# Kernel optimization log

Hardware: AMD Instinct MI355X
Metric: run time of the kernel (lower is better)

The kernel has to match this reference:

```python
import jax, jax.numpy as jnp
import numpy as np

B, K, D = 8, 256, 768      # batch, num proposals, appearance_feature_dim
DK = 96                    # key_feature_dim
DG = 96                    # geo_feature_dim
NR = 8                     # n_relations (NR*DK == D required by residual add)


def setup_inputs() -> dict:
    key = jax.random.key(0)
    ks = jax.random.split(key, 10)
    s = 0.02
    return {
        "f_a": jax.random.normal(ks[0], (B, K, D), jnp.float32),
        "position_embedding": jax.random.uniform(ks[1], (B, K, K, DG), jnp.float32),
        # stacked per-head parameters (NR heads)
        "WG_w": jax.random.normal(ks[2], (NR, DG), jnp.float32) * s,
        "WG_b": jnp.zeros((NR,), jnp.float32),
        "WK_w": jax.random.normal(ks[3], (NR, D, DK), jnp.float32) * s,
        "WK_b": jnp.zeros((NR, DK), jnp.float32),
        "WQ_w": jax.random.normal(ks[4], (NR, D, DK), jnp.float32) * s,
        "WQ_b": jnp.zeros((NR, DK), jnp.float32),
        "WV_w": jax.random.normal(ks[5], (NR, D, DK), jnp.float32) * s,
        "WV_b": jnp.zeros((NR, DK), jnp.float32),
    }


def reference(f_a, position_embedding, WG_w, WG_b, WK_w, WK_b, WQ_w, WQ_b, WV_w, WV_b):
    # Per-head projections, all heads at once: [B, H, K, DK]
    k = jnp.einsum('bkd,hde->bhke', f_a, WK_w) + WK_b[:, None, :]
    q = jnp.einsum('bkd,hde->bhke', f_a, WQ_w) + WQ_b[:, None, :]
    v = jnp.einsum('bkd,hde->bhke', f_a, WV_w) + WV_b[:, None, :]
    # scaled_dot[b,h,m,n] = <k_m, q_n> / sqrt(DK)  (matches w_k.view(B,K,1,dk)*w_q.view(B,1,K,dk))
    scores = jnp.einsum('bhme,bhne->bhmn', k, q) * (1.0 / np.sqrt(DK)).astype(np.float32)
    # geometric bias: relu(WG(pe)) -> [B,H,K,K]
    w_g = jax.nn.relu(jnp.einsum('bmng,hg->bhmn', position_embedding, WG_w) + WG_b[:, None, None])
    logits = jnp.log(jnp.clip(w_g, 1e-6)) + scores
    # torch Softmax(dim=1) on [B,K,K] -> normalize over m axis (axis=2 here)
    attn = jax.nn.softmax(logits, axis=2)
    # output[b,n,:] = sum_m attn[b,h,m,n] * v[b,h,m,:], heads concatenated on feature dim
    out = jnp.einsum('bhmn,bhmd->bnhd', attn, v).reshape(f_a.shape[0], f_a.shape[1], -1)
    return out + f_a  # concat + f_a residual from RelationalProposalModule
```

## Files before the change

### kernel.cpp

```cpp
#include <hip/hip_runtime.h>

#define DD   768
#define NH   8
#define DKh  96

typedef __attribute__((ext_vector_type(8))) short short8;
typedef __attribute__((ext_vector_type(4))) float f32x4;

__device__ __forceinline__ unsigned short f2bf(float x) {
    union { float f; unsigned int u; } v; v.f = x;
    unsigned int r = v.u + 0x7FFFu + ((v.u >> 16) & 1u);
    return (unsigned short)(r >> 16);
}

__global__ __launch_bounds__(256) void k_cvt_a(const float* __restrict__ fa,
                                               unsigned short* __restrict__ abf) {
    int idx = blockIdx.x * 256 + threadIdx.x;
    float4 v = ((const float4*)fa)[idx];
    ushort4 o;
    o.x = f2bf(v.x); o.y = f2bf(v.y); o.z = f2bf(v.z); o.w = f2bf(v.w);
    ((ushort4*)abf)[idx] = o;
}

__global__ __launch_bounds__(256) void k_cvt_w(const float* __restrict__ wk,
                                               const float* __restrict__ wq,
                                               const float* __restrict__ wv,
                                               unsigned short* __restrict__ wbf) {
    __shared__ float ls[64 * 97];
    int pid = blockIdx.x / 12;
    int db  = blockIdx.x % 12;
    int p = pid >> 3, h = pid & 7;
    const float* src = (p == 0 ? wk : p == 1 ? wq : wv) + h * DD * DKh + db * 64 * DKh;
    int t = threadIdx.x;
#pragma unroll
    for (int i = 0; i < 24; ++i) {
        int f = t + 256 * i;
        int dl = f / 96, e = f - dl * 96;
        ls[dl * 97 + e] = src[f];
    }
    __syncthreads();
    unsigned short* dst = wbf + (p * 768 + h * 96) * DD + db * 64;
#pragma unroll
    for (int i = 0; i < 24; ++i) {
        int f = t + 256 * i;
        int e = f >> 6, dl = f & 63;
        dst[e * DD + dl] = f2bf(ls[dl * 97 + e]);
    }
}

__global__ __launch_bounds__(256) void k_proj(const unsigned short* __restrict__ abf,
                                              const unsigned short* __restrict__ wbf,
                                              const float* __restrict__ wkb,
                                              const float* __restrict__ wqb,
                                              const float* __restrict__ wvb,
                                              unsigned short* __restrict__ kb,
                                              unsigned short* __restrict__ qb,
                                              unsigned short* __restrict__ vt) {
    int w = threadIdx.x >> 6, lane = threadIdx.x & 63;
    int lrow = lane & 15, quad = lane >> 4;
    int rt = blockIdx.x / 36, cg = blockIdx.x % 36;
    int r0 = rt * 64 + w * 16;
    int c0 = cg * 64;
    f32x4 z = {0.f, 0.f, 0.f, 0.f};
    f32x4 acc[4] = {z, z, z, z};
    for (int kk = 0; kk < DD; kk += 32) {
        short8 a = *(const short8*)(abf + (r0 + lrow) * DD + kk + quad * 8);
#pragma unroll
        for (int tt = 0; tt < 4; ++tt) {
            short8 b = *(const short8*)(wbf + (c0 + tt * 16 + lrow) * DD + kk + quad * 8);
            acc[tt] = __builtin_amdgcn_mfma_f32_16x16x32_bf16(a, b, acc[tt], 0, 0, 0);
        }
    }
    int rbase = r0 + quad * 4;
    int b_ = rbase >> 8, mbase = rbase & 255;
#pragma unroll
    for (int tt = 0; tt < 4; ++tt) {
        int cc = c0 + tt * 16 + lrow;
        int p = cc / 768, rm = cc - p * 768;
        int h = rm / 96,  e = rm - h * 96;
        float bias = (p == 0 ? wkb : p == 1 ? wqb : wvb)[h * 96 + e];
        if (p == 2) {
            ushort4 v4;
            v4.x = f2bf(acc[tt][0] + bias);
            v4.y = f2bf(acc[tt][1] + bias);
            v4.z = f2bf(acc[tt][2] + bias);
            v4.w = f2bf(acc[tt][3] + bias);
            *(ushort4*)(vt + ((b_ * 8 + h) * 96 + e) * 256 + mbase) = v4;
        } else {
            float sc = (p == 1) ? 0.10206207261596577f : 1.0f;
            unsigned short* dst = (p == 0 ? kb : qb) + ((b_ * 8 + h) * 256 + mbase) * 96 + e;
#pragma unroll
            for (int r = 0; r < 4; ++r)
                dst[r * 96] = f2bf((acc[tt][r] + bias) * sc);
        }
    }
}

__global__ __launch_bounds__(256) void k_wg(const float* __restrict__ pe,
                                            const float* __restrict__ wgw,
                                            const float* __restrict__ wgb,
                                            float* __restrict__ L) {
    int tid = blockIdx.x * 256 + threadIdx.x;
    int n = tid & 255, m = (tid >> 8) & 255, b = tid >> 16;
    const float4* row = (const float4*)(pe + (size_t)tid * 96);
    float acc[8];
#pragma unroll
    for (int h = 0; h < 8; ++h) acc[h] = wgb[h];
#pragma unroll
    for (int g4 = 0; g4 < 24; ++g4) {
        float4 v = row[g4];
#pragma unroll
        for (int h = 0; h < 8; ++h) {
            acc[h] = fmaf(v.x, wgw[h * 96 + g4 * 4 + 0], acc[h]);
            acc[h] = fmaf(v.y, wgw[h * 96 + g4 * 4 + 1], acc[h]);
            acc[h] = fmaf(v.z, wgw[h * 96 + g4 * 4 + 2], acc[h]);
            acc[h] = fmaf(v.w, wgw[h * 96 + g4 * 4 + 3], acc[h]);
        }
    }
    int base = (b * 8 * 256 + m) * 256 + n;
#pragma unroll
    for (int h = 0; h < 8; ++h)
        L[base + h * 65536] = __logf(fmaxf(acc[h], 1e-6f));
}

__global__ __launch_bounds__(256) void k_score(const unsigned short* __restrict__ kb,
                                               const unsigned short* __restrict__ qb,
                                               float* __restrict__ L) {
    int w = threadIdx.x >> 6, lane = threadIdx.x & 63;
    int lrow = lane & 15, quad = lane >> 4;
    int tid = blockIdx.x * 4 + w;
    int bh = tid >> 8, rem = tid & 255;
    int mt = rem >> 4, nt = rem & 15;
    int m0 = mt * 16, n0 = nt * 16;
    f32x4 acc = {0.f, 0.f, 0.f, 0.f};
    const unsigned short* ka = kb + (bh * 256 + m0 + lrow) * 96 + quad * 8;
    const unsigned short* qa = qb + (bh * 256 + n0 + lrow) * 96 + quad * 8;
#pragma unroll
    for (int kk = 0; kk < 96; kk += 32) {
        short8 a = *(const short8*)(ka + kk);
        short8 b = *(const short8*)(qa + kk);
        acc = __builtin_amdgcn_mfma_f32_16x16x32_bf16(a, b, acc, 0, 0, 0);
    }
    float* lp = L + (bh * 256 + m0 + quad * 4) * 256 + n0 + lrow;
#pragma unroll
    for (int r = 0; r < 4; ++r)
        lp[r * 256] += acc[r];
}

__global__ __launch_bounds__(256) void k_softmax(const float* __restrict__ L,
                                                 unsigned short* __restrict__ pt) {
    __shared__ float Ps[32 * 264];
    __shared__ float inv_s[32];
    int bh = blockIdx.x >> 3, nbk = blockIdx.x & 7;
    int n0 = nbk * 32;
    int t = threadIdx.x;
    int nl = t >> 3, j = t & 7;
    const float* base = L + bh * 65536 + n0 + nl;
    float mx = -3.4e38f;
    for (int m0 = 0; m0 < 256; m0 += 8)
        mx = fmaxf(mx, base[(m0 + j) * 256]);
    mx = fmaxf(mx, __shfl_xor(mx, 1));
    mx = fmaxf(mx, __shfl_xor(mx, 2));
    mx = fmaxf(mx, __shfl_xor(mx, 4));
    float sum = 0.f;
    for (int m0 = 0; m0 < 256; m0 += 8) {
        float v = base[(m0 + j) * 256];
        float e = __expf(v - mx);
        sum += e;
        Ps[nl * 264 + m0 + j] = e;
    }
    sum += __shfl_xor(sum, 1);
    sum += __shfl_xor(sum, 2);
    sum += __shfl_xor(sum, 4);
    if (j == 0) inv_s[nl] = 1.0f / sum;
    __syncthreads();
    unsigned short* dst = pt + (bh * 256 + n0) * 256;
#pragma unroll 4
    for (int i = 0; i < 32; ++i)
        dst[i * 256 + t] = f2bf(Ps[i * 264 + t] * inv_s[i]);
}

__global__ __launch_bounds__(256) void k_attnv(const unsigned short* __restrict__ pt,
                                               const unsigned short* __restrict__ vt,
                                               const float* __restrict__ fa,
                                               float* __restrict__ out) {
    int w = threadIdx.x >> 6, lane = threadIdx.x & 63;
    int lrow = lane & 15, quad = lane >> 4;
    int tid = blockIdx.x * 4 + w;
    int bh = tid / 96, rem = tid - bh * 96;
    int nt = rem / 6, et = rem - nt * 6;
    int n0 = nt * 16, e0 = et * 16;
    int b_ = bh >> 3, h = bh & 7;
    f32x4 acc = {0.f, 0.f, 0.f, 0.f};
    const unsigned short* pa = pt + (bh * 256 + n0 + lrow) * 256 + quad * 8;
    const unsigned short* va = vt + (bh * 96 + e0 + lrow) * 256 + quad * 8;
#pragma unroll
    for (int mk = 0; mk < 256; mk += 32) {
        short8 a = *(const short8*)(pa + mk);
        short8 b = *(const short8*)(va + mk);
        acc = __builtin_amdgcn_mfma_f32_16x16x32_bf16(a, b, acc, 0, 0, 0);
    }
    int idx = (b_ * 256 + n0 + quad * 4) * 768 + h * 96 + e0 + lrow;
#pragma unroll
    for (int r = 0; r < 4; ++r)
        out[idx + r * 768] = acc[r] + fa[idx + r * 768];
}

extern "C" void kernel_launch(void* const* d_in, const int* in_sizes, int n_in,
                              void* d_out, int out_size, void* d_ws, size_t ws_size,
                              hipStream_t stream) {
    const float* fa  = (const float*)d_in[0];
    const float* pe  = (const float*)d_in[1];
    const float* wgw = (const float*)d_in[2];
    const float* wgb = (const float*)d_in[3];
    const float* wkw = (const float*)d_in[4];
    const float* wkb = (const float*)d_in[5];
    const float* wqw = (const float*)d_in[6];
    const float* wqb = (const float*)d_in[7];
    const float* wvw = (const float*)d_in[8];
    const float* wvb = (const float*)d_in[9];
    float* out = (float*)d_out;
    char* ws = (char*)d_ws;
    unsigned short* abf = (unsigned short*)(ws);
    unsigned short* wbf = (unsigned short*)(ws + 3145728);
    unsigned short* kb  = (unsigned short*)(ws + 6684672);
    unsigned short* qb  = (unsigned short*)(ws + 9830400);
    unsigned short* vt  = (unsigned short*)(ws + 12976128);
    float*          L   = (float*)(ws + 16121856);
    unsigned short* pt  = (unsigned short*)(ws + 32899072);

    k_cvt_a  <<<1536, 256, 0, stream>>>(fa, abf);
    k_cvt_w  <<< 288, 256, 0, stream>>>(wkw, wqw, wvw, wbf);
    k_proj   <<<1152, 256, 0, stream>>>(abf, wbf, wkb, wqb, wvb, kb, qb, vt);
    k_wg     <<<2048, 256, 0, stream>>>(pe, wgw, wgb, L);
    k_score  <<<4096, 256, 0, stream>>>(kb, qb, L);
    k_softmax<<< 512, 256, 0, stream>>>(L, pt);
    k_attnv  <<<1536, 256, 0, stream>>>(pt, vt, fa, out);
}
```

Measured before the change: 419.5 us.

## Fuse geometric bias and score GEMM into one kernel using MFMA for WG

Merges the position-embedding projection and the QK score kernel into a single kernel that tiles 16x16 (m,n) blocks per batch. The WG projection is now done with bf16 MFMA after staging the pe tile in LDS, and the log bias is held in shared memory and added when the scores are written. This drops the write-then-read-modify-write round trip of the large L buffer and replaces scalar FMA loops with matrix instructions. In exchange the pe inputs lose precision to bf16 and each block uses about 58KB of LDS, which limits occupancy.

```diff
diff --git a/kernel.cpp b/kernel.cpp
--- a/kernel.cpp
+++ b/kernel.cpp
@@ -96,55 +96,76 @@
     }
 }
 
-__global__ __launch_bounds__(256) void k_wg(const float* __restrict__ pe,
-                                            const float* __restrict__ wgw,
-                                            const float* __restrict__ wgb,
-                                            float* __restrict__ L) {
-    int tid = blockIdx.x * 256 + threadIdx.x;
-    int n = tid & 255, m = (tid >> 8) & 255, b = tid >> 16;
-    const float4* row = (const float4*)(pe + (size_t)tid * 96);
-    float acc[8];
-#pragma unroll
-    for (int h = 0; h < 8; ++h) acc[h] = wgb[h];
-#pragma unroll
-    for (int g4 = 0; g4 < 24; ++g4) {
-        float4 v = row[g4];
-#pragma unroll
-        for (int h = 0; h < 8; ++h) {
-            acc[h] = fmaf(v.x, wgw[h * 96 + g4 * 4 + 0], acc[h]);
-            acc[h] = fmaf(v.y, wgw[h * 96 + g4 * 4 + 1], acc[h]);
-            acc[h] = fmaf(v.z, wgw[h * 96 + g4 * 4 + 2], acc[h]);
-            acc[h] = fmaf(v.w, wgw[h * 96 + g4 * 4 + 3], acc[h]);
-        }
-    }
-    int base = (b * 8 * 256 + m) * 256 + n;
-#pragma unroll
-    for (int h = 0; h < 8; ++h)
-        L[base + h * 65536] = __logf(fmaxf(acc[h], 1e-6f));
-}
-
-__global__ __launch_bounds__(256) void k_score(const unsigned short* __restrict__ kb,
-                                               const unsigned short* __restrict__ qb,
-                                               float* __restrict__ L) {
-    int w = threadIdx.x >> 6, lane = threadIdx.x & 63;
-    int lrow = lane & 15, quad = lane >> 4;
-    int tid = blockIdx.x * 4 + w;
-    int bh = tid >> 8, rem = tid & 255;
-    int mt = rem >> 4, nt = rem & 15;
+__global__ __launch_bounds__(256) void k_wgs(const float* __restrict__ pe,
+                                             const float* __restrict__ wgw,
+                                             const float* __restrict__ wgb,
+                                             const unsigned short* __restrict__ kb,
+                                             const unsigned short* __restrict__ qb,
+                                             float* __restrict__ L) {
+    __shared__ unsigned short peb[256 * 96];
+    __shared__ unsigned short wgl[16 * 96];
+    __shared__ float stot[8 * 256];
+    int bi = blockIdx.x;
+    int b = bi >> 8, mt = (bi >> 4) & 15, nt = bi & 15;
     int m0 = mt * 16, n0 = nt * 16;
-    f32x4 acc = {0.f, 0.f, 0.f, 0.f};
-    const unsigned short* ka = kb + (bh * 256 + m0 + lrow) * 96 + quad * 8;
-    const unsigned short* qa = qb + (bh * 256 + n0 + lrow) * 96 + quad * 8;
-#pragma unroll
-    for (int kk = 0; kk < 96; kk += 32) {
-        short8 a = *(const short8*)(ka + kk);
-        short8 b = *(const short8*)(qa + kk);
-        acc = __builtin_amdgcn_mfma_f32_16x16x32_bf16(a, b, acc, 0, 0, 0);
-    }
-    float* lp = L + (bh * 256 + m0 + quad * 4) * 256 + n0 + lrow;
-#pragma unroll
-    for (int r = 0; r < 4; ++r)
-        lp[r * 256] += acc[r];
+    int t = threadIdx.x;
+#pragma unroll
+    for (int i = 0; i < 6; ++i) {
+        int f = t + 256 * i;
+        int c = f / 96, k = f - c * 96;
+        wgl[f] = (c < 8) ? f2bf(wgw[c * 96 + k]) : (unsigned short)0;
+    }
+    const float* peg = pe + ((size_t)(b * 256 + m0) * 256 + n0) * 96;
+#pragma unroll
+    for (int i = 0; i < 24; ++i) {
+        int f = t + 256 * i;
+        int mi = f / 384, rem = f - mi * 384;
+        float4 v = *(const float4*)(peg + (size_t)mi * 24576 + rem * 4);
+        ushort4 o;
+        o.x = f2bf(v.x); o.y = f2bf(v.y); o.z = f2bf(v.z); o.w = f2bf(v.w);
+        *(ushort4*)(peb + mi * 1536 + rem * 4) = o;
+    }
+    __syncthreads();
+    int w = t >> 6, lane = t & 63, lrow = lane & 15, quad = lane >> 4;
+    short8 bf[3];
+#pragma unroll
+    for (int ks = 0; ks < 3; ++ks)
+        bf[ks] = *(const short8*)(wgl + lrow * 96 + ks * 32 + quad * 8);
+    float gbias = wgb[lrow & 7];
+#pragma unroll
+    for (int rt4 = 0; rt4 < 4; ++rt4) {
+        int rt = w * 4 + rt4;
+        f32x4 acc = {0.f, 0.f, 0.f, 0.f};
+#pragma unroll
+        for (int ks = 0; ks < 3; ++ks) {
+            short8 a = *(const short8*)(peb + (rt * 16 + lrow) * 96 + ks * 32 + quad * 8);
+            acc = __builtin_amdgcn_mfma_f32_16x16x32_bf16(a, bf[ks], acc, 0, 0, 0);
+        }
+        if (lrow < 8) {
+#pragma unroll
+            for (int r = 0; r < 4; ++r)
+                stot[lrow * 256 + rt * 16 + quad * 4 + r] =
+                    __logf(fmaxf(acc[r] + gbias, 1e-6f));
+        }
+    }
+    __syncthreads();
+#pragma unroll
+    for (int hh = 0; hh < 2; ++hh) {
+        int h = w * 2 + hh;
+        const unsigned short* ka = kb + ((size_t)((b * 8 + h) * 256) + m0 + lrow) * 96 + quad * 8;
+        const unsigned short* qa = qb + ((size_t)((b * 8 + h) * 256) + n0 + lrow) * 96 + quad * 8;
+        f32x4 acc = {0.f, 0.f, 0.f, 0.f};
+#pragma unroll
+        for (int ks = 0; ks < 3; ++ks) {
+            short8 a  = *(const short8*)(ka + ks * 32);
+            short8 bq = *(const short8*)(qa + ks * 32);
+            acc = __builtin_amdgcn_mfma_f32_16x16x32_bf16(a, bq, acc, 0, 0, 0);
+        }
+        float* lp = L + ((size_t)((b * 8 + h) * 256) + m0 + quad * 4) * 256 + n0 + lrow;
+#pragma unroll
+        for (int r = 0; r < 4; ++r)
+            lp[r * 256] = acc[r] + stot[h * 256 + (quad * 4 + r) * 16 + lrow];
+    }
 }
 
 __global__ __launch_bounds__(256) void k_softmax(const float* __restrict__ L,
@@ -232,8 +253,7 @@
     k_cvt_a  <<<1536, 256, 0, stream>>>(fa, abf);
     k_cvt_w  <<< 288, 256, 0, stream>>>(wkw, wqw, wvw, wbf);
     k_proj   <<<1152, 256, 0, stream>>>(abf, wbf, wkb, wqb, wvb, kb, qb, vt);
-    k_wg     <<<2048, 256, 0, stream>>>(pe, wgw, wgb, L);
-    k_score  <<<4096, 256, 0, stream>>>(kb, qb, L);
+    k_wgs    <<<2048, 256, 0, stream>>>(pe, wgw, wgb, kb, qb, L);
     k_softmax<<< 512, 256, 0, stream>>>(L, pt);
     k_attnv  <<<1536, 256, 0, stream>>>(pt, vt, fa, out);
 }
```

Measured after the change: 406.0 us. 3.2% less time.
